# Optimization experiments

Measured on AMD Instinct MI355X. Metric: run time of the kernel, lower is better.

Reference implementation:

```python
import jax, jax.numpy as jnp
import numpy as np

LATENT = 256
HIDDEN = 512
NODE_F = 128
MAX_NODES = 50
B = 128


def _mk_linear(key, fan_in, fan_out):
    kw, kb = jax.random.split(key)
    bound = 1.0 / np.sqrt(fan_in)
    W = jax.random.uniform(kw, (fan_in, fan_out), jnp.float32, -bound, bound)
    b = jax.random.uniform(kb, (fan_out,), jnp.float32, -bound, bound)
    return W, b


def setup_inputs() -> dict:
    key = jax.random.key(0)
    ks = jax.random.split(key, 7)
    z = jax.random.normal(ks[0], (B, LATENT), jnp.float32)
    # node decoder: latent -> hidden -> hidden -> max_nodes*node_features
    nw1, nb1 = _mk_linear(ks[1], LATENT, HIDDEN)
    nw2, nb2 = _mk_linear(ks[2], HIDDEN, HIDDEN)
    nw3, nb3 = _mk_linear(ks[3], HIDDEN, MAX_NODES * NODE_F)
    # edge decoder: latent + 2*node_features -> hidden -> hidden//2 -> 1
    ew1, eb1 = _mk_linear(ks[4], LATENT + 2 * NODE_F, HIDDEN)
    ew2, eb2 = _mk_linear(ks[5], HIDDEN, HIDDEN // 2)
    ew3, eb3 = _mk_linear(ks[6], HIDDEN // 2, 1)
    return {"z": z,
            "nw1": nw1, "nb1": nb1, "nw2": nw2, "nb2": nb2, "nw3": nw3, "nb3": nb3,
            "ew1": ew1, "eb1": eb1, "ew2": ew2, "eb2": eb2, "ew3": ew3, "eb3": eb3}


def reference(z, nw1, nb1, nw2, nb2, nw3, nb3, ew1, eb1, ew2, eb2, ew3, eb3):
    # ---- node decoder ----
    h = jax.nn.relu(z @ nw1 + nb1)
    h = jax.nn.relu(h @ nw2 + nb2)
    node_logits = h @ nw3 + nb3                      # [B, MAX_NODES*NODE_F]
    node_feats = node_logits.reshape(z.shape[0], MAX_NODES, NODE_F)
    node_probs = jax.nn.sigmoid(node_feats)

    # ---- edge decoder: vectorize the O(N^2) python loop over upper-tri pairs ----
    # jnp.triu_indices matches the torch loop order: i ascending, j ascending per i.
    ii, jj = jnp.triu_indices(MAX_NODES, k=1)        # [P] each, P = 1225
    ni = node_feats[:, ii, :]                        # [B, P, NODE_F]
    nj = node_feats[:, jj, :]                        # [B, P, NODE_F]
    zb = jnp.broadcast_to(z[:, None, :], (z.shape[0], ii.shape[0], z.shape[1]))
    edge_in = jnp.concatenate([zb, ni, nj], axis=-1)  # [B, P, LATENT+2*NODE_F]
    e = jax.nn.relu(edge_in @ ew1 + eb1)             # [B, P, HIDDEN]
    e = jax.nn.relu(e @ ew2 + eb2)                   # [B, P, HIDDEN//2]
    edge_probs = jax.nn.sigmoid(e @ ew3 + eb3)[..., 0]  # [B, P]
    return node_probs, edge_probs
```

## Files before the change

### kernel.cpp

```cpp
#include <hip/hip_runtime.h>
#include <hip/hip_bf16.h>
#include <math.h>

#define LATENT 256
#define HIDDEN 512
#define NODE_F 128
#define MAX_NODES 50
#define NPAIRS 1225
#define BATCH 128
#define NODE_OUT 6400
#define MTILE 64
#define TPB 10
#define EDGE_BLOCKS 256

typedef __attribute__((ext_vector_type(8))) short short8;
typedef __attribute__((ext_vector_type(4))) float float4v;

union S8U { short8 s; unsigned int u[4]; };

__device__ __forceinline__ float bf2f(ushort u) {
    union { unsigned int i; float f; } v; v.i = ((unsigned int)u) << 16; return v.f;
}
__device__ __forceinline__ ushort f2bf(float f) {
    union { unsigned int i; float f; } v; v.f = f;
    unsigned int r = v.i + 0x7fffu + ((v.i >> 16) & 1u);
    return (ushort)(r >> 16);
}
__device__ __forceinline__ unsigned int pk_bf16(float f0, float f1) {
    __hip_bfloat162 p = __float22bfloat162_rn(float2{f0, f1});
    unsigned int w; __builtin_memcpy(&w, &p, 4); return w;
}
__device__ __forceinline__ float sigmoidf(float x) {
    return 1.0f / (1.0f + __expf(-x));
}

#define TR3_B0   0
#define PREP_B0  800
#define ZC_B0    1824
#define ND_B0    2080
#define PT_B0    2336
#define PREPK_NB 2341

__global__ __launch_bounds__(256) void k_prep_all(
    const float* __restrict__ nw3, ushort* __restrict__ nw3T,
    const float* __restrict__ ew1, const float* __restrict__ ew2,
    ushort* __restrict__ ew2T, ushort* __restrict__ wijT,
    const float* __restrict__ z, const float* __restrict__ eb1,
    float* __restrict__ Zc,
    const float* __restrict__ nw1, const float* __restrict__ nb1,
    const float* __restrict__ nw2, const float* __restrict__ nb2,
    ushort* __restrict__ h2b, int* __restrict__ ptab)
{
    __shared__ float smem[64 * 65];
    int b = blockIdx.x;
    int tid = threadIdx.x;

    if (b < PREP_B0) {
        int bb = b - TR3_B0;
        int k0 = (bb & 7) * 64;
        int n0 = (bb >> 3) * 64;
        int tx = tid & 63, ty = tid >> 6;
#pragma unroll
        for (int r = 0; r < 16; r++) {
            int row = r * 4 + ty;
            smem[row * 65 + tx] = nw3[(k0 + row) * NODE_OUT + n0 + tx];
        }
        __syncthreads();
#pragma unroll
        for (int c = 0; c < 16; c++) {
            int n = c * 4 + ty;
            nw3T[(size_t)(n0 + n) * HIDDEN + k0 + tx] = f2bf(smem[tx * 65 + n]);
        }
    } else if (b < ZC_B0) {
        int t = (b - PREP_B0) * 256 + tid;
        if (t < 256 * 512) {
            int n = t >> 9, k = t & 511;
            ew2T[t] = f2bf(ew2[k * 256 + n]);
        } else {
            int u = t - 256 * 512;
            int n = u >> 7, k = u & 127;
            float s = (n < 512) ? ew1[(256 + k) * 512 + n] : ew1[(384 + k) * 512 + (n - 512)];
            wijT[u] = f2bf(s);
        }
    } else if (b < ND_B0) {
        int b2 = b - ZC_B0;
        int r = b2 >> 1, o = (b2 & 1) * 256 + tid;
        float* zs = smem;
        zs[tid] = z[r * LATENT + tid];
        __syncthreads();
        float acc = 0.f;
#pragma unroll 8
        for (int k = 0; k < LATENT; k++) acc += zs[k] * ew1[k * HIDDEN + o];
        Zc[r * HIDDEN + o] = acc + eb1[o];
    } else if (b < PT_B0) {
        int b2 = b - ND_B0;
        int r = b2 >> 1, half = b2 & 1;
        float* zs = smem;
        float* hs = smem + 256;
        zs[tid] = z[r * LATENT + tid];
        __syncthreads();
        float a0 = 0.f, a1 = 0.f;
#pragma unroll 8
        for (int k = 0; k < LATENT; k++) {
            float zk = zs[k];
            a0 += zk * nw1[k * HIDDEN + tid];
            a1 += zk * nw1[k * HIDDEN + tid + 256];
        }
        hs[tid]       = fmaxf(a0 + nb1[tid], 0.f);
        hs[tid + 256] = fmaxf(a1 + nb1[tid + 256], 0.f);
        __syncthreads();
        int o = half * 256 + tid;
        float acc = 0.f;
#pragma unroll 8
        for (int k = 0; k < HIDDEN; k++) acc += hs[k] * nw2[k * HIDDEN + o];
        acc += nb2[o];
        h2b[r * HIDDEN + o] = f2bf(fmaxf(acc, 0.f));
    } else {
        int p = (b - PT_B0) * 256 + tid;
        if (p < NPAIRS) {
            int i = 0, off = 0;
            while (p - off >= MAX_NODES - 1 - i) { off += MAX_NODES - 1 - i; ++i; }
            int j = i + 1 + (p - off);
            ptab[p] = (i << 8) | j;
        }
    }
}

__global__ __launch_bounds__(256, 4) void k_node_out_mfma(
    const ushort* __restrict__ h2b, const ushort* __restrict__ nw3T,
    const float* __restrict__ nb3, float* __restrict__ node_probs,
    ushort* __restrict__ node_feats)
{
    int tid = threadIdx.x;
    int wave = tid >> 6, lane = tid & 63;
    int m16 = lane & 15, quad = lane >> 4;
    int n0 = (blockIdx.x >> 1) * 64;
    int m0 = (blockIdx.x & 1) * 64;
    int col = n0 + wave * 16 + m16;

    float4v acc[4];
#pragma unroll
    for (int mt = 0; mt < 4; mt++) acc[mt] = (float4v)(0.f);

    const ushort* bb = nw3T + (size_t)col * HIDDEN;
#pragma unroll
    for (int it = 0; it < 16; ++it) {
        int kk = it * 32 + quad * 8;
        short8 b = *(const short8*)(bb + kk);
#pragma unroll
        for (int mt = 0; mt < 4; mt++) {
            short8 a = *(const short8*)(h2b + (m0 + mt * 16 + m16) * HIDDEN + kk);
            acc[mt] = __builtin_amdgcn_mfma_f32_16x16x32_bf16(a, b, acc[mt], 0, 0, 0);
        }
    }
    float bias = nb3[col];
#pragma unroll
    for (int mt = 0; mt < 4; mt++)
#pragma unroll
        for (int t = 0; t < 4; t++) {
            int row = m0 + mt * 16 + quad * 4 + t;
            float v = acc[mt][t] + bias;
            node_probs[(size_t)row * NODE_OUT + col] = sigmoidf(v);
            node_feats[(size_t)row * NODE_OUT + col] = f2bf(v);
        }
}

__global__ __launch_bounds__(256, 4) void k_uv(
    const ushort* __restrict__ nf, const ushort* __restrict__ wijT,
    ushort* __restrict__ UV)
{
    int tid = threadIdx.x;
    int wave = tid >> 6, lane = tid & 63;
    int m16 = lane & 15, quad = lane >> 4;
    int bm = blockIdx.x >> 2, bn = blockIdx.x & 3;
    int base = bn * 256 + wave * 64;
    int r0 = bm * 64;

    float4v acc[4][4];
#pragma unroll
    for (int mt = 0; mt < 4; mt++)
#pragma unroll
        for (int nt = 0; nt < 4; nt++) acc[mt][nt] = (float4v)(0.f);

#pragma unroll
    for (int k0 = 0; k0 < NODE_F; k0 += 32) {
        int kk = k0 + quad * 8;
        short8 a0 = *(const short8*)(nf + (r0 + m16) * NODE_F + kk);
        short8 a1 = *(const short8*)(nf + (r0 + 16 + m16) * NODE_F + kk);
        short8 a2 = *(const short8*)(nf + (r0 + 32 + m16) * NODE_F + kk);
        short8 a3 = *(const short8*)(nf + (r0 + 48 + m16) * NODE_F + kk);
#pragma unroll
        for (int nt = 0; nt < 4; nt++) {
            int n = base + nt * 16 + m16;
            short8 b = *(const short8*)(wijT + n * NODE_F + kk);
            acc[0][nt] = __builtin_amdgcn_mfma_f32_16x16x32_bf16(a0, b, acc[0][nt], 0, 0, 0);
            acc[1][nt] = __builtin_amdgcn_mfma_f32_16x16x32_bf16(a1, b, acc[1][nt], 0, 0, 0);
            acc[2][nt] = __builtin_amdgcn_mfma_f32_16x16x32_bf16(a2, b, acc[2][nt], 0, 0, 0);
            acc[3][nt] = __builtin_amdgcn_mfma_f32_16x16x32_bf16(a3, b, acc[3][nt], 0, 0, 0);
        }
    }
#pragma unroll
    for (int nt = 0; nt < 4; nt++) {
        int colg = base + nt * 16 + m16;
#pragma unroll
        for (int mt = 0; mt < 4; mt++)
#pragma unroll
            for (int t = 0; t < 4; t++) {
                int rr = r0 + mt * 16 + quad * 4 + t;
                UV[(size_t)rr * 1024 + colg] = f2bf(acc[mt][nt][t]);
            }
    }
}

__global__ __launch_bounds__(512, 2) void k_edge8(
    const float* __restrict__ Zc, const ushort* __restrict__ UV,
    const ushort* __restrict__ ew2T, const float* __restrict__ ew3,
    const float* __restrict__ eb2, const float* __restrict__ eb3,
    const int* __restrict__ ptab, float* __restrict__ out_edges)
{
    __shared__ __align__(16) ushort h1[2][MTILE][HIDDEN + 8];
    __shared__ float part[MTILE][8];
    __shared__ int uo5[TPB][MTILE], vo5[TPB][MTILE];

    int tid  = threadIdx.x;
    int blk  = blockIdx.x;
    int b    = blk >> 1;
    int ti0  = (blk & 1) * TPB;

    if (tid < MTILE) {
#pragma unroll
        for (int t = 0; t < TPB; t++) {
            int p = (ti0 + t) * MTILE + tid;
            if (p >= NPAIRS) p = NPAIRS - 1;
            int ij = ptab[p];
            uo5[t][tid] = (b * MAX_NODES + (ij >> 8)) * 1024;
            vo5[t][tid] = (b * MAX_NODES + (ij & 255)) * 1024 + 512;
        }
    }

    int wave = tid >> 6, lane = tid & 63;
    int m16 = lane & 15, quad = lane >> 4;
    int c8 = lane * 8;
    int kk0 = quad * 8;

    float4v zA = *(const float4v*)(Zc + b * HIDDEN + c8);
    float4v zB = *(const float4v*)(Zc + b * HIDDEN + c8 + 4);

    const ushort* bb0 = ew2T + (wave * 32 + m16) * HIDDEN;
    const ushort* bb1 = ew2T + (wave * 32 + 16 + m16) * HIDDEN;
    short8 Breg[16][2];
#pragma unroll
    for (int kc = 0; kc < 16; kc++) {
        Breg[kc][0] = *(const short8*)(bb0 + kc * 32 + kk0);
        Breg[kc][1] = *(const short8*)(bb1 + kc * 32 + kk0);
    }
    float eb2v[2], ew3v[2];
    eb2v[0] = eb2[wave * 32 + m16];      eb2v[1] = eb2[wave * 32 + 16 + m16];
    ew3v[0] = ew3[wave * 32 + m16];      ew3v[1] = ew3[wave * 32 + 16 + m16];

    __syncthreads();

#pragma unroll
    for (int rr = 0; rr < 8; rr++) {
        int r = wave * 8 + rr;
        short8 u8 = *(const short8*)(UV + uo5[0][r] + c8);
        short8 v8 = *(const short8*)(UV + vo5[0][r] + c8);
        S8U hh;
#pragma unroll
        for (int e2 = 0; e2 < 4; e2++) {
            float z0 = (e2 < 2) ? zA[e2 * 2] : zB[e2 * 2 - 4];
            float z1 = (e2 < 2) ? zA[e2 * 2 + 1] : zB[e2 * 2 - 3];
            float f0 = fmaxf(z0 + bf2f((ushort)u8[e2 * 2]) + bf2f((ushort)v8[e2 * 2]), 0.f);
            float f1 = fmaxf(z1 + bf2f((ushort)u8[e2 * 2 + 1]) + bf2f((ushort)v8[e2 * 2 + 1]), 0.f);
            hh.u[e2] = pk_bf16(f0, f1);
        }
        *(short8*)&h1[0][r][c8] = hh.s;
    }
    __syncthreads();

    for (int t = 0; t < TPB; t++) {
        int cur = t & 1, nxt = cur ^ 1;
        bool hasNext = (t + 1 < TPB);

        float4v acc2[4][2];
#pragma unroll
        for (int mt = 0; mt < 4; mt++)
#pragma unroll
            for (int nt = 0; nt < 2; nt++) acc2[mt][nt] = (float4v)(0.f);

        short8 uu[4], vv[4];
        if (hasNext) {
#pragma unroll
            for (int rr = 0; rr < 4; rr++) {
                int r = wave * 8 + rr;
                uu[rr] = *(const short8*)(UV + uo5[t + 1][r] + c8);
                vv[rr] = *(const short8*)(UV + vo5[t + 1][r] + c8);
            }
        }
#pragma unroll
        for (int it = 0; it < 8; ++it) {
            int kk = it * 32 + kk0;
            short8 a0 = *(const short8*)&h1[cur][m16][kk];
            short8 a1 = *(const short8*)&h1[cur][16 + m16][kk];
            short8 a2 = *(const short8*)&h1[cur][32 + m16][kk];
            short8 a3 = *(const short8*)&h1[cur][48 + m16][kk];
            acc2[0][0] = __builtin_amdgcn_mfma_f32_16x16x32_bf16(a0, Breg[it][0], acc2[0][0], 0, 0, 0);
            acc2[1][0] = __builtin_amdgcn_mfma_f32_16x16x32_bf16(a1, Breg[it][0], acc2[1][0], 0, 0, 0);
            acc2[2][0] = __builtin_amdgcn_mfma_f32_16x16x32_bf16(a2, Breg[it][0], acc2[2][0], 0, 0, 0);
            acc2[3][0] = __builtin_amdgcn_mfma_f32_16x16x32_bf16(a3, Breg[it][0], acc2[3][0], 0, 0, 0);
            acc2[0][1] = __builtin_amdgcn_mfma_f32_16x16x32_bf16(a0, Breg[it][1], acc2[0][1], 0, 0, 0);
            acc2[1][1] = __builtin_amdgcn_mfma_f32_16x16x32_bf16(a1, Breg[it][1], acc2[1][1], 0, 0, 0);
            acc2[2][1] = __builtin_amdgcn_mfma_f32_16x16x32_bf16(a2, Breg[it][1], acc2[2][1], 0, 0, 0);
            acc2[3][1] = __builtin_amdgcn_mfma_f32_16x16x32_bf16(a3, Breg[it][1], acc2[3][1], 0, 0, 0);
        }
        if (hasNext) {
#pragma unroll
            for (int rr = 0; rr < 4; rr++) {
                int r = wave * 8 + rr;
                S8U hh;
#pragma unroll
                for (int e2 = 0; e2 < 4; e2++) {
                    float z0 = (e2 < 2) ? zA[e2 * 2] : zB[e2 * 2 - 4];
                    float z1 = (e2 < 2) ? zA[e2 * 2 + 1] : zB[e2 * 2 - 3];
                    float f0 = fmaxf(z0 + bf2f((ushort)uu[rr][e2 * 2]) + bf2f((ushort)vv[rr][e2 * 2]), 0.f);
                    float f1 = fmaxf(z1 + bf2f((ushort)uu[rr][e2 * 2 + 1]) + bf2f((ushort)vv[rr][e2 * 2 + 1]), 0.f);
                    hh.u[e2] = pk_bf16(f0, f1);
                }
                *(short8*)&h1[nxt][r][c8] = hh.s;
            }
#pragma unroll
            for (int rr = 0; rr < 4; rr++) {
                int r = wave * 8 + 4 + rr;
                uu[rr] = *(const short8*)(UV + uo5[t + 1][r] + c8);
                vv[rr] = *(const short8*)(UV + vo5[t + 1][r] + c8);
            }
        }
#pragma unroll
        for (int it = 8; it < 16; ++it) {
            int kk = it * 32 + kk0;
            short8 a0 = *(const short8*)&h1[cur][m16][kk];
            short8 a1 = *(const short8*)&h1[cur][16 + m16][kk];
            short8 a2 = *(const short8*)&h1[cur][32 + m16][kk];
            short8 a3 = *(const short8*)&h1[cur][48 + m16][kk];
            acc2[0][0] = __builtin_amdgcn_mfma_f32_16x16x32_bf16(a0, Breg[it][0], acc2[0][0], 0, 0, 0);
            acc2[1][0] = __builtin_amdgcn_mfma_f32_16x16x32_bf16(a1, Breg[it][0], acc2[1][0], 0, 0, 0);
            acc2[2][0] = __builtin_amdgcn_mfma_f32_16x16x32_bf16(a2, Breg[it][0], acc2[2][0], 0, 0, 0);
            acc2[3][0] = __builtin_amdgcn_mfma_f32_16x16x32_bf16(a3, Breg[it][0], acc2[3][0], 0, 0, 0);
            acc2[0][1] = __builtin_amdgcn_mfma_f32_16x16x32_bf16(a0, Breg[it][1], acc2[0][1], 0, 0, 0);
            acc2[1][1] = __builtin_amdgcn_mfma_f32_16x16x32_bf16(a1, Breg[it][1], acc2[1][1], 0, 0, 0);
            acc2[2][1] = __builtin_amdgcn_mfma_f32_16x16x32_bf16(a2, Breg[it][1], acc2[2][1], 0, 0, 0);
            acc2[3][1] = __builtin_amdgcn_mfma_f32_16x16x32_bf16(a3, Breg[it][1], acc2[3][1], 0, 0, 0);
        }
        if (hasNext) {
#pragma unroll
            for (int rr = 0; rr < 4; rr++) {
                int r = wave * 8 + 4 + rr;
                S8U hh;
#pragma unroll
                for (int e2 = 0; e2 < 4; e2++) {
                    float z0 = (e2 < 2) ? zA[e2 * 2] : zB[e2 * 2 - 4];
                    float z1 = (e2 < 2) ? zA[e2 * 2 + 1] : zB[e2 * 2 - 3];
                    float f0 = fmaxf(z0 + bf2f((ushort)uu[rr][e2 * 2]) + bf2f((ushort)vv[rr][e2 * 2]), 0.f);
                    float f1 = fmaxf(z1 + bf2f((ushort)uu[rr][e2 * 2 + 1]) + bf2f((ushort)vv[rr][e2 * 2 + 1]), 0.f);
                    hh.u[e2] = pk_bf16(f0, f1);
                }
                *(short8*)&h1[nxt][r][c8] = hh.s;
            }
        }

#pragma unroll
        for (int mt = 0; mt < 4; mt++)
#pragma unroll
            for (int tt = 0; tt < 4; tt++) {
                float s = 0.f;
#pragma unroll
                for (int nt = 0; nt < 2; nt++)
                    s += fmaxf(acc2[mt][nt][tt] + eb2v[nt], 0.f) * ew3v[nt];
                s += __shfl_xor(s, 1);
                s += __shfl_xor(s, 2);
                s += __shfl_xor(s, 4);
                s += __shfl_xor(s, 8);
                if (m16 == 0) part[mt * 16 + quad * 4 + tt][wave] = s;
            }
        __syncthreads();

        if (tid < MTILE) {
            int p = (ti0 + t) * MTILE + tid;
            if (p < NPAIRS) {
                float v = eb3[0];
#pragma unroll
                for (int w = 0; w < 8; w++) v += part[tid][w];
                out_edges[b * NPAIRS + p] = sigmoidf(v);
            }
        }
        __syncthreads();
    }
}

extern "C" void kernel_launch(void* const* d_in, const int* in_sizes, int n_in,
                              void* d_out, int out_size, void* d_ws, size_t ws_size,
                              hipStream_t stream) {
    const float* z   = (const float*)d_in[0];
    const float* nw1 = (const float*)d_in[1];
    const float* nb1 = (const float*)d_in[2];
    const float* nw2 = (const float*)d_in[3];
    const float* nb2 = (const float*)d_in[4];
    const float* nw3 = (const float*)d_in[5];
    const float* nb3 = (const float*)d_in[6];
    const float* ew1 = (const float*)d_in[7];
    const float* eb1 = (const float*)d_in[8];
    const float* ew2 = (const float*)d_in[9];
    const float* eb2 = (const float*)d_in[10];
    const float* ew3 = (const float*)d_in[11];
    const float* eb3 = (const float*)d_in[12];

    char* ws = (char*)d_ws;
    int*    ptab = (int*)(ws);
    ushort* h2b  = (ushort*)(ws + 262144);
    ushort* nf   = (ushort*)(ws + 393216);
    ushort* ew2T = (ushort*)(ws + 2031616);
    ushort* wijT = (ushort*)(ws + 2293760);
    ushort* nw3T = (ushort*)(ws + 2555904);
    float*  Zc   = (float*)(ws + 9109504);
    ushort* UV   = (ushort*)(ws + 9371648);

    float* out_nodes = (float*)d_out;
    float* out_edges = out_nodes + BATCH * NODE_OUT;

    k_prep_all<<<PREPK_NB, 256, 0, stream>>>(nw3, nw3T, ew1, ew2, ew2T, wijT,
                                             z, eb1, Zc, nw1, nb1, nw2, nb2,
                                             h2b, ptab);
    k_node_out_mfma<<<200, 256, 0, stream>>>(h2b, nw3T, nb3, out_nodes, nf);
    k_uv<<<400, 256, 0, stream>>>(nf, wijT, UV);
    k_edge8<<<EDGE_BLOCKS, 512, 0, stream>>>(Zc, UV, ew2T, ew3,
                                             eb2, eb3, ptab, out_edges);
}
```

Before: 225.8 us.

## Fuse four kernel launches into one cooperative persistent kernel with grid syncs

Replaces the four-launch sequence (prep, node output GEMM, UV projection, edge MLP) with a single cooperative kernel of 256 blocks that runs each stage in turn, separated by grid-wide barriers. This removes launch gaps and per-kernel tail effects. In exchange the early stages run on fewer blocks and threads than their dedicated kernels had, and each grid sync costs something. If the cooperative launch fails, the old multi-kernel path runs instead.

```diff
diff --git a/kernel.cpp b/kernel.cpp
--- a/kernel.cpp
+++ b/kernel.cpp
@@ -1,6 +1,9 @@
 #include <hip/hip_runtime.h>
 #include <hip/hip_bf16.h>
+#include <hip/hip_cooperative_groups.h>
 #include <math.h>
+
+namespace cg = cooperative_groups;
 
 #define LATENT 256
 #define HIDDEN 512
@@ -11,7 +14,8 @@
 #define NODE_OUT 6400
 #define MTILE 64
 #define TPB 10
-#define EDGE_BLOCKS 256
+#define NBLK 256
+#define NTHR 512
 
 typedef __attribute__((ext_vector_type(8))) short short8;
 typedef __attribute__((ext_vector_type(4))) float float4v;
@@ -32,6 +36,340 @@
 }
 __device__ __forceinline__ float sigmoidf(float x) {
     return 1.0f / (1.0f + __expf(-x));
+}
+
+__global__ __launch_bounds__(512, 2) void k_all(
+    const float* __restrict__ z,   const float* __restrict__ nw1, const float* __restrict__ nb1,
+    const float* __restrict__ nw2, const float* __restrict__ nb2, const float* __restrict__ nw3,
+    const float* __restrict__ nb3, const float* __restrict__ ew1, const float* __restrict__ eb1,
+    const float* __restrict__ ew2, const float* __restrict__ eb2, const float* __restrict__ ew3,
+    const float* __restrict__ eb3,
+    int* __restrict__ ptab, ushort* __restrict__ h2b, ushort* __restrict__ nf,
+    ushort* __restrict__ ew2T, ushort* __restrict__ wijT, ushort* __restrict__ nw3T,
+    float* __restrict__ Zc, ushort* __restrict__ UV,
+    float* __restrict__ node_probs, float* __restrict__ out_edges)
+{
+    __shared__ __align__(16) char lds[140288];
+    cg::grid_group gg = cg::this_grid();
+
+    int tid = threadIdx.x;
+    int blk = blockIdx.x;
+    int wave = tid >> 6, lane = tid & 63;
+    int m16 = lane & 15, quad = lane >> 4;
+
+    for (int t = blk * NTHR + tid; t < 131072 + 131072 + NPAIRS; t += NBLK * NTHR) {
+        if (t < 131072) {
+            int n = t >> 9, k = t & 511;
+            ew2T[t] = f2bf(ew2[k * 256 + n]);
+        } else if (t < 262144) {
+            int u = t - 131072;
+            int n = u >> 7, k = u & 127;
+            float s = (n < 512) ? ew1[(256 + k) * 512 + n] : ew1[(384 + k) * 512 + (n - 512)];
+            wijT[u] = f2bf(s);
+        } else {
+            int p = t - 262144;
+            int i = 0, off = 0;
+            while (p - off >= MAX_NODES - 1 - i) { off += MAX_NODES - 1 - i; ++i; }
+            ptab[p] = (i << 8) | (i + 1 + (p - off));
+        }
+    }
+    {
+        float* smem = (float*)lds;
+        for (int j = blk; j < 1056; j += NBLK) {
+            if (j < 800) {
+                int k0 = (j & 7) * 64;
+                int n0 = (j >> 3) * 64;
+                int tx = tid & 63, ty = tid >> 6;
+#pragma unroll
+                for (int r = 0; r < 8; r++) {
+                    int row = r * 8 + ty;
+                    smem[row * 65 + tx] = nw3[(k0 + row) * NODE_OUT + n0 + tx];
+                }
+                __syncthreads();
+#pragma unroll
+                for (int c = 0; c < 8; c++) {
+                    int n = c * 8 + ty;
+                    nw3T[(size_t)(n0 + n) * HIDDEN + k0 + tx] = f2bf(smem[tx * 65 + n]);
+                }
+            } else if (j < 928) {
+                int r = j - 800;
+                if (tid < 256) smem[tid] = z[r * LATENT + tid];
+                __syncthreads();
+                float acc = 0.f;
+#pragma unroll 8
+                for (int k = 0; k < LATENT; k++) acc += smem[k] * ew1[k * HIDDEN + tid];
+                Zc[r * HIDDEN + tid] = acc + eb1[tid];
+            } else {
+                int r = j - 928;
+                float* hs = smem + 256;
+                if (tid < 256) smem[tid] = z[r * LATENT + tid];
+                __syncthreads();
+                float a = 0.f;
+#pragma unroll 8
+                for (int k = 0; k < LATENT; k++) a += smem[k] * nw1[k * HIDDEN + tid];
+                hs[tid] = fmaxf(a + nb1[tid], 0.f);
+                __syncthreads();
+                float acc = 0.f;
+#pragma unroll 8
+                for (int k = 0; k < HIDDEN; k++) acc += hs[k] * nw2[k * HIDDEN + tid];
+                h2b[r * HIDDEN + tid] = f2bf(fmaxf(acc + nb2[tid], 0.f));
+            }
+            __syncthreads();
+        }
+    }
+    gg.sync();
+
+    if (blk < 100) {
+        int n0 = blk * 64;
+        int col = n0 + (wave & 3) * 16 + m16;
+        int m0 = (wave >> 2) * 64;
+
+        float4v acc[4];
+#pragma unroll
+        for (int mt = 0; mt < 4; mt++) acc[mt] = (float4v)(0.f);
+
+        const ushort* bb = nw3T + (size_t)col * HIDDEN;
+#pragma unroll
+        for (int it = 0; it < 16; ++it) {
+            int kk = it * 32 + quad * 8;
+            short8 b = *(const short8*)(bb + kk);
+#pragma unroll
+            for (int mt = 0; mt < 4; mt++) {
+                short8 a = *(const short8*)(h2b + (m0 + mt * 16 + m16) * HIDDEN + kk);
+                acc[mt] = __builtin_amdgcn_mfma_f32_16x16x32_bf16(a, b, acc[mt], 0, 0, 0);
+            }
+        }
+        float bias = nb3[col];
+#pragma unroll
+        for (int mt = 0; mt < 4; mt++)
+#pragma unroll
+            for (int t = 0; t < 4; t++) {
+                int row = m0 + mt * 16 + quad * 4 + t;
+                float v = acc[mt][t] + bias;
+                node_probs[(size_t)row * NODE_OUT + col] = sigmoidf(v);
+                nf[(size_t)row * NODE_OUT + col] = f2bf(v);
+            }
+    }
+    gg.sync();
+
+    if (blk < 200) {
+        int bm = blk >> 1, bn = blk & 1;
+        int base = bn * 512 + wave * 64;
+        int r0 = bm * 64;
+
+        float4v acc[4][4];
+#pragma unroll
+        for (int mt = 0; mt < 4; mt++)
+#pragma unroll
+            for (int nt = 0; nt < 4; nt++) acc[mt][nt] = (float4v)(0.f);
+
+#pragma unroll
+        for (int k0 = 0; k0 < NODE_F; k0 += 32) {
+            int kk = k0 + quad * 8;
+            short8 a0 = *(const short8*)(nf + (r0 + m16) * NODE_F + kk);
+            short8 a1 = *(const short8*)(nf + (r0 + 16 + m16) * NODE_F + kk);
+            short8 a2 = *(const short8*)(nf + (r0 + 32 + m16) * NODE_F + kk);
+            short8 a3 = *(const short8*)(nf + (r0 + 48 + m16) * NODE_F + kk);
+#pragma unroll
+            for (int nt = 0; nt < 4; nt++) {
+                int n = base + nt * 16 + m16;
+                short8 b = *(const short8*)(wijT + n * NODE_F + kk);
+                acc[0][nt] = __builtin_amdgcn_mfma_f32_16x16x32_bf16(a0, b, acc[0][nt], 0, 0, 0);
+                acc[1][nt] = __builtin_amdgcn_mfma_f32_16x16x32_bf16(a1, b, acc[1][nt], 0, 0, 0);
+                acc[2][nt] = __builtin_amdgcn_mfma_f32_16x16x32_bf16(a2, b, acc[2][nt], 0, 0, 0);
+                acc[3][nt] = __builtin_amdgcn_mfma_f32_16x16x32_bf16(a3, b, acc[3][nt], 0, 0, 0);
+            }
+        }
+#pragma unroll
+        for (int nt = 0; nt < 4; nt++) {
+            int colg = base + nt * 16 + m16;
+#pragma unroll
+            for (int mt = 0; mt < 4; mt++)
+#pragma unroll
+                for (int t = 0; t < 4; t++) {
+                    int rr = r0 + mt * 16 + quad * 4 + t;
+                    UV[(size_t)rr * 1024 + colg] = f2bf(acc[mt][nt][t]);
+                }
+        }
+    }
+    gg.sync();
+
+    {
+        ushort (*h1)[MTILE][HIDDEN + 8] = (ushort (*)[MTILE][HIDDEN + 8])lds;
+        float (*partE)[8] = (float (*)[8])(lds + 133120);
+        int (*uo5)[MTILE] = (int (*)[MTILE])(lds + 135168);
+        int (*vo5)[MTILE] = (int (*)[MTILE])(lds + 137728);
+
+        int b   = blk >> 1;
+        int ti0 = (blk & 1) * TPB;
+
+        if (tid < MTILE) {
+#pragma unroll
+            for (int t = 0; t < TPB; t++) {
+                int p = (ti0 + t) * MTILE + tid;
+                if (p >= NPAIRS) p = NPAIRS - 1;
+                int ij = ptab[p];
+                uo5[t][tid] = (b * MAX_NODES + (ij >> 8)) * 1024;
+                vo5[t][tid] = (b * MAX_NODES + (ij & 255)) * 1024 + 512;
+            }
+        }
+
+        int c8 = lane * 8;
+        int kk0 = quad * 8;
+
+        float4v zA = *(const float4v*)(Zc + b * HIDDEN + c8);
+        float4v zB = *(const float4v*)(Zc + b * HIDDEN + c8 + 4);
+
+        const ushort* bb0 = ew2T + (wave * 32 + m16) * HIDDEN;
+        const ushort* bb1 = ew2T + (wave * 32 + 16 + m16) * HIDDEN;
+        short8 Breg[16][2];
+#pragma unroll
+        for (int kc = 0; kc < 16; kc++) {
+            Breg[kc][0] = *(const short8*)(bb0 + kc * 32 + kk0);
+            Breg[kc][1] = *(const short8*)(bb1 + kc * 32 + kk0);
+        }
+        float eb2v[2], ew3v[2];
+        eb2v[0] = eb2[wave * 32 + m16];      eb2v[1] = eb2[wave * 32 + 16 + m16];
+        ew3v[0] = ew3[wave * 32 + m16];      ew3v[1] = ew3[wave * 32 + 16 + m16];
+
+        __syncthreads();
+
+#pragma unroll
+        for (int rr = 0; rr < 8; rr++) {
+            int r = wave * 8 + rr;
+            short8 u8 = *(const short8*)(UV + uo5[0][r] + c8);
+            short8 v8 = *(const short8*)(UV + vo5[0][r] + c8);
+            S8U hh;
+#pragma unroll
+            for (int e2 = 0; e2 < 4; e2++) {
+                float z0 = (e2 < 2) ? zA[e2 * 2] : zB[e2 * 2 - 4];
+                float z1 = (e2 < 2) ? zA[e2 * 2 + 1] : zB[e2 * 2 - 3];
+                float f0 = fmaxf(z0 + bf2f((ushort)u8[e2 * 2]) + bf2f((ushort)v8[e2 * 2]), 0.f);
+                float f1 = fmaxf(z1 + bf2f((ushort)u8[e2 * 2 + 1]) + bf2f((ushort)v8[e2 * 2 + 1]), 0.f);
+                hh.u[e2] = pk_bf16(f0, f1);
+            }
+            *(short8*)&h1[0][r][c8] = hh.s;
+        }
+        __syncthreads();
+
+        for (int t = 0; t < TPB; t++) {
+            int cur = t & 1, nxt = cur ^ 1;
+            bool hasNext = (t + 1 < TPB);
+
+            float4v acc2[4][2];
+#pragma unroll
+            for (int mt = 0; mt < 4; mt++)
+#pragma unroll
+                for (int nt = 0; nt < 2; nt++) acc2[mt][nt] = (float4v)(0.f);
+
+            short8 uu[4], vv[4];
+            if (hasNext) {
+#pragma unroll
+                for (int rr = 0; rr < 4; rr++) {
+                    int r = wave * 8 + rr;
+                    uu[rr] = *(const short8*)(UV + uo5[t + 1][r] + c8);
+                    vv[rr] = *(const short8*)(UV + vo5[t + 1][r] + c8);
+                }
+            }
+#pragma unroll
+            for (int it = 0; it < 8; ++it) {
+                int kk = it * 32 + kk0;
+                short8 a0 = *(const short8*)&h1[cur][m16][kk];
+                short8 a1 = *(const short8*)&h1[cur][16 + m16][kk];
+                short8 a2 = *(const short8*)&h1[cur][32 + m16][kk];
+                short8 a3 = *(const short8*)&h1[cur][48 + m16][kk];
+                acc2[0][0] = __builtin_amdgcn_mfma_f32_16x16x32_bf16(a0, Breg[it][0], acc2[0][0], 0, 0, 0);
+                acc2[1][0] = __builtin_amdgcn_mfma_f32_16x16x32_bf16(a1, Breg[it][0], acc2[1][0], 0, 0, 0);
+                acc2[2][0] = __builtin_amdgcn_mfma_f32_16x16x32_bf16(a2, Breg[it][0], acc2[2][0], 0, 0, 0);
+                acc2[3][0] = __builtin_amdgcn_mfma_f32_16x16x32_bf16(a3, Breg[it][0], acc2[3][0], 0, 0, 0);
+                acc2[0][1] = __builtin_amdgcn_mfma_f32_16x16x32_bf16(a0, Breg[it][1], acc2[0][1], 0, 0, 0);
+                acc2[1][1] = __builtin_amdgcn_mfma_f32_16x16x32_bf16(a1, Breg[it][1], acc2[1][1], 0, 0, 0);
+                acc2[2][1] = __builtin_amdgcn_mfma_f32_16x16x32_bf16(a2, Breg[it][1], acc2[2][1], 0, 0, 0);
+                acc2[3][1] = __builtin_amdgcn_mfma_f32_16x16x32_bf16(a3, Breg[it][1], acc2[3][1], 0, 0, 0);
+            }
+            if (hasNext) {
+#pragma unroll
+                for (int rr = 0; rr < 4; rr++) {
+                    int r = wave * 8 + rr;
+                    S8U hh;
+#pragma unroll
+                    for (int e2 = 0; e2 < 4; e2++) {
+                        float z0 = (e2 < 2) ? zA[e2 * 2] : zB[e2 * 2 - 4];
+                        float z1 = (e2 < 2) ? zA[e2 * 2 + 1] : zB[e2 * 2 - 3];
+                        float f0 = fmaxf(z0 + bf2f((ushort)uu[rr][e2 * 2]) + bf2f((ushort)vv[rr][e2 * 2]), 0.f);
+                        float f1 = fmaxf(z1 + bf2f((ushort)uu[rr][e2 * 2 + 1]) + bf2f((ushort)vv[rr][e2 * 2 + 1]), 0.f);
+                        hh.u[e2] = pk_bf16(f0, f1);
+                    }
+                    *(short8*)&h1[nxt][r][c8] = hh.s;
+                }
+#pragma unroll
+                for (int rr = 0; rr < 4; rr++) {
+                    int r = wave * 8 + 4 + rr;
+                    uu[rr] = *(const short8*)(UV + uo5[t + 1][r] + c8);
+                    vv[rr] = *(const short8*)(UV + vo5[t + 1][r] + c8);
+                }
+            }
+#pragma unroll
+            for (int it = 8; it < 16; ++it) {
+                int kk = it * 32 + kk0;
+                short8 a0 = *(const short8*)&h1[cur][m16][kk];
+                short8 a1 = *(const short8*)&h1[cur][16 + m16][kk];
+                short8 a2 = *(const short8*)&h1[cur][32 + m16][kk];
+                short8 a3 = *(const short8*)&h1[cur][48 + m16][kk];
+                acc2[0][0] = __builtin_amdgcn_mfma_f32_16x16x32_bf16(a0, Breg[it][0], acc2[0][0], 0, 0, 0);
+                acc2[1][0] = __builtin_amdgcn_mfma_f32_16x16x32_bf16(a1, Breg[it][0], acc2[1][0], 0, 0, 0);
+                acc2[2][0] = __builtin_amdgcn_mfma_f32_16x16x32_bf16(a2, Breg[it][0], acc2[2][0], 0, 0, 0);
+                acc2[3][0] = __builtin_amdgcn_mfma_f32_16x16x32_bf16(a3, Breg[it][0], acc2[3][0], 0, 0, 0);
+                acc2[0][1] = __builtin_amdgcn_mfma_f32_16x16x32_bf16(a0, Breg[it][1], acc2[0][1], 0, 0, 0);
+                acc2[1][1] = __builtin_amdgcn_mfma_f32_16x16x32_bf16(a1, Breg[it][1], acc2[1][1], 0, 0, 0);
+                acc2[2][1] = __builtin_amdgcn_mfma_f32_16x16x32_bf16(a2, Breg[it][1], acc2[2][1], 0, 0, 0);
+                acc2[3][1] = __builtin_amdgcn_mfma_f32_16x16x32_bf16(a3, Breg[it][1], acc2[3][1], 0, 0, 0);
+            }
+            if (hasNext) {
+#pragma unroll
+                for (int rr = 0; rr < 4; rr++) {
+                    int r = wave * 8 + 4 + rr;
+                    S8U hh;
+#pragma unroll
+                    for (int e2 = 0; e2 < 4; e2++) {
+                        float z0 = (e2 < 2) ? zA[e2 * 2] : zB[e2 * 2 - 4];
+                        float z1 = (e2 < 2) ? zA[e2 * 2 + 1] : zB[e2 * 2 - 3];
+                        float f0 = fmaxf(z0 + bf2f((ushort)uu[rr][e2 * 2]) + bf2f((ushort)vv[rr][e2 * 2]), 0.f);
+                        float f1 = fmaxf(z1 + bf2f((ushort)uu[rr][e2 * 2 + 1]) + bf2f((ushort)vv[rr][e2 * 2 + 1]), 0.f);
+                        hh.u[e2] = pk_bf16(f0, f1);
+                    }
+                    *(short8*)&h1[nxt][r][c8] = hh.s;
+                }
+            }
+
+#pragma unroll
+            for (int mt = 0; mt < 4; mt++)
+#pragma unroll
+                for (int tt = 0; tt < 4; tt++) {
+                    float s = 0.f;
+#pragma unroll
+                    for (int nt = 0; nt < 2; nt++)
+                        s += fmaxf(acc2[mt][nt][tt] + eb2v[nt], 0.f) * ew3v[nt];
+                    s += __shfl_xor(s, 1);
+                    s += __shfl_xor(s, 2);
+                    s += __shfl_xor(s, 4);
+                    s += __shfl_xor(s, 8);
+                    if (m16 == 0) partE[mt * 16 + quad * 4 + tt][wave] = s;
+                }
+            __syncthreads();
+
+            if (tid < MTILE) {
+                int p = (ti0 + t) * MTILE + tid;
+                if (p < NPAIRS) {
+                    float v = eb3[0];
+#pragma unroll
+                    for (int w = 0; w < 8; w++) v += partE[tid][w];
+                    out_edges[b * NPAIRS + p] = sigmoidf(v);
+                }
+            }
+            __syncthreads();
+        }
+    }
 }
 
 #define TR3_B0   0
@@ -427,11 +765,22 @@
     float* out_nodes = (float*)d_out;
     float* out_edges = out_nodes + BATCH * NODE_OUT;
 
-    k_prep_all<<<PREPK_NB, 256, 0, stream>>>(nw3, nw3T, ew1, ew2, ew2T, wijT,
-                                             z, eb1, Zc, nw1, nb1, nw2, nb2,
-                                             h2b, ptab);
-    k_node_out_mfma<<<200, 256, 0, stream>>>(h2b, nw3T, nb3, out_nodes, nf);
-    k_uv<<<400, 256, 0, stream>>>(nf, wijT, UV);
-    k_edge8<<<EDGE_BLOCKS, 512, 0, stream>>>(Zc, UV, ew2T, ew3,
-                                             eb2, eb3, ptab, out_edges);
-}
+    void* args[] = {
+        (void*)&z, (void*)&nw1, (void*)&nb1, (void*)&nw2, (void*)&nb2,
+        (void*)&nw3, (void*)&nb3, (void*)&ew1, (void*)&eb1, (void*)&ew2,
+        (void*)&eb2, (void*)&ew3, (void*)&eb3,
+        (void*)&ptab, (void*)&h2b, (void*)&nf, (void*)&ew2T, (void*)&wijT,
+        (void*)&nw3T, (void*)&Zc, (void*)&UV, (void*)&out_nodes, (void*)&out_edges
+    };
+    hipError_t e = hipLaunchCooperativeKernel((void*)k_all, dim3(NBLK), dim3(NTHR),
+                                              args, 0, stream);
+    if (e != hipSuccess) {
+        (void)hipGetLastError();
+        k_prep_all<<<PREPK_NB, 256, 0, stream>>>(nw3, nw3T, ew1, ew2, ew2T, wijT,
+                                                 z, eb1, Zc, nw1, nb1, nw2, nb2,
+                                                 h2b, ptab);
+        k_node_out_mfma<<<200, 256, 0, stream>>>(h2b, nw3T, nb3, out_nodes, nf);
+        k_uv<<<400, 256, 0, stream>>>(nf, wijT, UV);
+        k_edge8<<<NBLK, 512, 0, stream>>>(Zc, UV, ew2T, ew3, eb2, eb3, ptab, out_edges);
+    }
+}
```

Result: slower. 332.7 us (+47.4%).

## Fuse node-output GEMM with UV projection through shared memory

Applied to the files above, without the earlier changes.

Merges the node-logit GEMM and the per-node UV projection into one kernel. Each block computes a 16-row by one-node (128-feature) slice of node logits, writes the sigmoid probabilities out, keeps the bf16 features in shared memory, and then multiplies them by the edge weights to produce the UV rows. This removes one launch and the global write/read of the node-feature buffer. In exchange, each block now re-reads the full wijT slice, the MFMA tiles are smaller with less reuse, and a block-wide sync sits between the two stages.

```diff
diff --git a/kernel.cpp b/kernel.cpp
--- a/kernel.cpp
+++ b/kernel.cpp
@@ -11,7 +11,7 @@
 #define NODE_OUT 6400
 #define MTILE 64
 #define TPB 10
-#define EDGE_BLOCKS 256
+#define NBLK 256
 
 typedef __attribute__((ext_vector_type(8))) short short8;
 typedef __attribute__((ext_vector_type(4))) float float4v;
@@ -126,89 +126,73 @@
     }
 }
 
-__global__ __launch_bounds__(256, 4) void k_node_out_mfma(
+__global__ __launch_bounds__(256, 2) void k_nodeuv(
     const ushort* __restrict__ h2b, const ushort* __restrict__ nw3T,
-    const float* __restrict__ nb3, float* __restrict__ node_probs,
-    ushort* __restrict__ node_feats)
+    const float* __restrict__ nb3, const ushort* __restrict__ wijT,
+    float* __restrict__ node_probs, ushort* __restrict__ UV)
 {
+    __shared__ ushort nf_s[16][136];
+
     int tid = threadIdx.x;
     int wave = tid >> 6, lane = tid & 63;
     int m16 = lane & 15, quad = lane >> 4;
-    int n0 = (blockIdx.x >> 1) * 64;
-    int m0 = (blockIdx.x & 1) * 64;
-    int col = n0 + wave * 16 + m16;
-
-    float4v acc[4];
-#pragma unroll
-    for (int mt = 0; mt < 4; mt++) acc[mt] = (float4v)(0.f);
-
-    const ushort* bb = nw3T + (size_t)col * HIDDEN;
+    int g  = blockIdx.x >> 3;
+    int m0 = (blockIdx.x & 7) * 16;
+
+    float4v accA[2];
+    accA[0] = (float4v)(0.f); accA[1] = (float4v)(0.f);
+
+    int colA0 = g * 128 + wave * 32 + m16;
+    const ushort* a0p = h2b + (m0 + m16) * HIDDEN;
+    const ushort* b0p = nw3T + (size_t)colA0 * HIDDEN;
+    const ushort* b1p = nw3T + (size_t)(colA0 + 16) * HIDDEN;
 #pragma unroll
     for (int it = 0; it < 16; ++it) {
         int kk = it * 32 + quad * 8;
-        short8 b = *(const short8*)(bb + kk);
-#pragma unroll
-        for (int mt = 0; mt < 4; mt++) {
-            short8 a = *(const short8*)(h2b + (m0 + mt * 16 + m16) * HIDDEN + kk);
-            acc[mt] = __builtin_amdgcn_mfma_f32_16x16x32_bf16(a, b, acc[mt], 0, 0, 0);
-        }
-    }
-    float bias = nb3[col];
-#pragma unroll
-    for (int mt = 0; mt < 4; mt++)
+        short8 a  = *(const short8*)(a0p + kk);
+        short8 b0 = *(const short8*)(b0p + kk);
+        short8 b1 = *(const short8*)(b1p + kk);
+        accA[0] = __builtin_amdgcn_mfma_f32_16x16x32_bf16(a, b0, accA[0], 0, 0, 0);
+        accA[1] = __builtin_amdgcn_mfma_f32_16x16x32_bf16(a, b1, accA[1], 0, 0, 0);
+    }
+#pragma unroll
+    for (int nt = 0; nt < 2; nt++) {
+        int col = colA0 + nt * 16;
+        float bias = nb3[col];
 #pragma unroll
         for (int t = 0; t < 4; t++) {
-            int row = m0 + mt * 16 + quad * 4 + t;
-            float v = acc[mt][t] + bias;
-            node_probs[(size_t)row * NODE_OUT + col] = sigmoidf(v);
-            node_feats[(size_t)row * NODE_OUT + col] = f2bf(v);
-        }
-}
-
-__global__ __launch_bounds__(256, 4) void k_uv(
-    const ushort* __restrict__ nf, const ushort* __restrict__ wijT,
-    ushort* __restrict__ UV)
-{
-    int tid = threadIdx.x;
-    int wave = tid >> 6, lane = tid & 63;
-    int m16 = lane & 15, quad = lane >> 4;
-    int bm = blockIdx.x >> 2, bn = blockIdx.x & 3;
-    int base = bn * 256 + wave * 64;
-    int r0 = bm * 64;
-
-    float4v acc[4][4];
-#pragma unroll
-    for (int mt = 0; mt < 4; mt++)
-#pragma unroll
-        for (int nt = 0; nt < 4; nt++) acc[mt][nt] = (float4v)(0.f);
-
-#pragma unroll
-    for (int k0 = 0; k0 < NODE_F; k0 += 32) {
-        int kk = k0 + quad * 8;
-        short8 a0 = *(const short8*)(nf + (r0 + m16) * NODE_F + kk);
-        short8 a1 = *(const short8*)(nf + (r0 + 16 + m16) * NODE_F + kk);
-        short8 a2 = *(const short8*)(nf + (r0 + 32 + m16) * NODE_F + kk);
-        short8 a3 = *(const short8*)(nf + (r0 + 48 + m16) * NODE_F + kk);
-#pragma unroll
-        for (int nt = 0; nt < 4; nt++) {
+            int row = quad * 4 + t;
+            float v = accA[nt][t] + bias;
+            node_probs[(size_t)(m0 + row) * NODE_OUT + col] = sigmoidf(v);
+            nf_s[row][wave * 32 + nt * 16 + m16] = f2bf(v);
+        }
+    }
+    __syncthreads();
+
+    float4v accB[16];
+#pragma unroll
+    for (int nt = 0; nt < 16; nt++) accB[nt] = (float4v)(0.f);
+
+    int base = wave * 256;
+#pragma unroll
+    for (int kit = 0; kit < 4; ++kit) {
+        int kk = kit * 32 + quad * 8;
+        short8 a = *(const short8*)&nf_s[m16][kk];
+#pragma unroll
+        for (int nt = 0; nt < 16; nt++) {
             int n = base + nt * 16 + m16;
             short8 b = *(const short8*)(wijT + n * NODE_F + kk);
-            acc[0][nt] = __builtin_amdgcn_mfma_f32_16x16x32_bf16(a0, b, acc[0][nt], 0, 0, 0);
-            acc[1][nt] = __builtin_amdgcn_mfma_f32_16x16x32_bf16(a1, b, acc[1][nt], 0, 0, 0);
-            acc[2][nt] = __builtin_amdgcn_mfma_f32_16x16x32_bf16(a2, b, acc[2][nt], 0, 0, 0);
-            acc[3][nt] = __builtin_amdgcn_mfma_f32_16x16x32_bf16(a3, b, acc[3][nt], 0, 0, 0);
-        }
-    }
-#pragma unroll
-    for (int nt = 0; nt < 4; nt++) {
+            accB[nt] = __builtin_amdgcn_mfma_f32_16x16x32_bf16(a, b, accB[nt], 0, 0, 0);
+        }
+    }
+#pragma unroll
+    for (int nt = 0; nt < 16; nt++) {
         int colg = base + nt * 16 + m16;
 #pragma unroll
-        for (int mt = 0; mt < 4; mt++)
-#pragma unroll
-            for (int t = 0; t < 4; t++) {
-                int rr = r0 + mt * 16 + quad * 4 + t;
-                UV[(size_t)rr * 1024 + colg] = f2bf(acc[mt][nt][t]);
-            }
+        for (int t = 0; t < 4; t++) {
+            int row = quad * 4 + t;
+            UV[((size_t)(m0 + row) * MAX_NODES + g) * 1024 + colg] = f2bf(accB[nt][t]);
+        }
     }
 }
 
@@ -417,7 +401,6 @@
     char* ws = (char*)d_ws;
     int*    ptab = (int*)(ws);
     ushort* h2b  = (ushort*)(ws + 262144);
-    ushort* nf   = (ushort*)(ws + 393216);
     ushort* ew2T = (ushort*)(ws + 2031616);
     ushort* wijT = (ushort*)(ws + 2293760);
     ushort* nw3T = (ushort*)(ws + 2555904);
@@ -430,8 +413,6 @@
     k_prep_all<<<PREPK_NB, 256, 0, stream>>>(nw3, nw3T, ew1, ew2, ew2T, wijT,
                                              z, eb1, Zc, nw1, nb1, nw2, nb2,
                                              h2b, ptab);
-    k_node_out_mfma<<<200, 256, 0, stream>>>(h2b, nw3T, nb3, out_nodes, nf);
-    k_uv<<<400, 256, 0, stream>>>(nf, wijT, UV);
-    k_edge8<<<EDGE_BLOCKS, 512, 0, stream>>>(Zc, UV, ew2T, ew3,
-                                             eb2, eb3, ptab, out_edges);
-}
+    k_nodeuv<<<400, 256, 0, stream>>>(h2b, nw3T, nb3, wijT, out_nodes, UV);
+    k_edge8<<<NBLK, 512, 0, stream>>>(Zc, UV, ew2T, ew3, eb2, eb3, ptab, out_edges);
+}
```

New measurement: 231.5 us. +2.5%, slower.
